# Kernel tuning notes

Hardware: AMD Instinct MI355X
Metric: run time of the kernel (lower is better)

Reference implementation:

```python
import jax, jax.numpy as jnp
import numpy as np

EPS = 1e-5  # torch InstanceNorm2d default eps


def setup_inputs() -> dict:
    key = jax.random.key(0)
    k1, k2, k3, k4, k5 = jax.random.split(key, 5)
    # shapes forced by the module: h*w == 64 (Linear(64,192)), (n,s,c) == (25,128,2)
    inp = jax.random.normal(k1, (25, 2, 128, 8, 8), dtype=jnp.float32)
    qkv_w = jax.random.normal(k2, (192, 64), dtype=jnp.float32) * 0.125
    qkv_b = jax.random.normal(k3, (192,), dtype=jnp.float32) * 0.02
    proj_w = jax.random.normal(k4, (64, 64), dtype=jnp.float32) * 0.125
    proj_b = jax.random.normal(k5, (64,), dtype=jnp.float32) * 0.02
    return {"inp": inp, "qkv_w": qkv_w, "qkv_b": qkv_b,
            "proj_w": proj_w, "proj_b": proj_b}


def reference(inp, qkv_w, qkv_b, proj_w, proj_b):
    n, c, s, h, w = inp.shape  # (25, 2, 128, 8, 8)
    hw = h * w  # 64
    # view(n,c,s,hw).transpose(1,2) -> (n, s, c, hw)
    x = jnp.transpose(inp.reshape(n, c, s, hw), (0, 2, 1, 3))
    # InstanceNorm2d(affine=False): normalize over the last two dims (c, hw)
    # per (n, s) instance, biased variance, eps=1e-5.
    mean = jnp.mean(x, axis=(2, 3), keepdims=True)
    var = jnp.var(x, axis=(2, 3), keepdims=True)
    x = (x - mean) * jax.lax.rsqrt(var + EPS)
    # fused QKV projection on the hw(=64) dim
    qkv = x @ qkv_w.T + qkv_b  # (n, s, c, 192)
    q, k, v = jnp.split(qkv, 3, axis=-1)  # each (n, s, c, 64)
    # linear attention: out = v + q @ (k^T @ v); the 'lower' branch in the
    # original is dead code (never used), so it is omitted.
    kv = jnp.einsum('nscd,nsce->nsde', k, v)  # (n, s, 64, 64)
    attn = v + jnp.einsum('nscd,nsde->nsce', q, kv)  # (n, s, c, 64)
    out = attn @ proj_w.T + proj_b  # dropout is identity in eval mode
    # transpose(1,2).reshape(n,c,s,h,w), residual, final merge of (c,s)
    out = jnp.transpose(out, (0, 2, 1, 3)).reshape(n, c, s, h, w)
    return (out + inp).reshape(n, c * s, h, w)
```

## Files before the change

kernel.cpp:

```cpp
#include <hip/hip_runtime.h>

#define EPS 1e-5f


typedef _Float16 half8 __attribute__((ext_vector_type(8)));
typedef _Float16 half4 __attribute__((ext_vector_type(4)));
typedef float    f32x4 __attribute__((ext_vector_type(4)));

__device__ __forceinline__ int swz(int row, int colByte) {
    return row * 128 + (colByte ^ ((row & 7) << 4));
}

__global__ __launch_bounds__(128)
void attn_mfma(const float* __restrict__ inp,
               const float* __restrict__ qkv_w,
               const float* __restrict__ qkv_b,
               const float* __restrict__ proj_w,
               const float* __restrict__ proj_b,
               float* __restrict__ out)
{
    __shared__ _Float16 w_lds[192 * 64];
    __shared__ _Float16 p_lds[64 * 64];
    __shared__ _Float16 a_lds[32 * 64];

    const int tid = threadIdx.x;
    const int w   = tid >> 6;
    const int l   = tid & 63;
    const int lr  = l & 15;
    const int lg  = l >> 4;

    #pragma unroll
    for (int k = 0; k < 24; ++k) {
        const int idx4 = tid + k * 128;
        const float4 v = reinterpret_cast<const float4*>(qkv_w)[idx4];
        const int row  = idx4 >> 4;
        const int colB = (idx4 & 15) * 8;
        half4 h = { (_Float16)v.x, (_Float16)v.y, (_Float16)v.z, (_Float16)v.w };
        *reinterpret_cast<half4*>(reinterpret_cast<char*>(w_lds) + swz(row, colB)) = h;
    }
    #pragma unroll
    for (int k = 0; k < 8; ++k) {
        const int idx4 = tid + k * 128;
        const float4 v = reinterpret_cast<const float4*>(proj_w)[idx4];
        const int row  = idx4 >> 4;
        const int colB = (idx4 & 15) * 8;
        half4 h = { (_Float16)v.x, (_Float16)v.y, (_Float16)v.z, (_Float16)v.w };
        *reinterpret_cast<half4*>(reinterpret_cast<char*>(p_lds) + swz(row, colB)) = h;
    }

    const int lrow = (w << 4) | lr;
    const int R    = blockIdx.x * 32 + lrow;
    const int g    = R >> 1;
    const int c    = R & 1;
    const int n    = g >> 7;
    const int s    = g & 127;
    const int rowbase = ((n * 2 + c) * 128 + s) * 64;
    const int col0 = lg * 8;

    const float4 x0a = *reinterpret_cast<const float4*>(inp + rowbase + col0);
    const float4 x0b = *reinterpret_cast<const float4*>(inp + rowbase + col0 + 4);
    const float4 x1a = *reinterpret_cast<const float4*>(inp + rowbase + col0 + 32);
    const float4 x1b = *reinterpret_cast<const float4*>(inp + rowbase + col0 + 36);

    float s1 = (x0a.x + x0a.y) + (x0a.z + x0a.w) + (x0b.x + x0b.y) + (x0b.z + x0b.w)
             + (x1a.x + x1a.y) + (x1a.z + x1a.w) + (x1b.x + x1b.y) + (x1b.z + x1b.w);
    float s2 = x0a.x*x0a.x + x0a.y*x0a.y + x0a.z*x0a.z + x0a.w*x0a.w
             + x0b.x*x0b.x + x0b.y*x0b.y + x0b.z*x0b.z + x0b.w*x0b.w
             + x1a.x*x1a.x + x1a.y*x1a.y + x1a.z*x1a.z + x1a.w*x1a.w
             + x1b.x*x1b.x + x1b.y*x1b.y + x1b.z*x1b.z + x1b.w*x1b.w;
    s1 += __shfl_xor(s1, 1);  s2 += __shfl_xor(s2, 1);
    s1 += __shfl_xor(s1, 16); s2 += __shfl_xor(s2, 16);
    s1 += __shfl_xor(s1, 32); s2 += __shfl_xor(s2, 32);
    const float mean = s1 * (1.0f / 128.0f);
    const float var  = s2 * (1.0f / 128.0f) - mean * mean;
    const float rs   = rsqrtf(var + EPS);

    half8 a0, a1;
    a0[0]=(_Float16)((x0a.x-mean)*rs); a0[1]=(_Float16)((x0a.y-mean)*rs);
    a0[2]=(_Float16)((x0a.z-mean)*rs); a0[3]=(_Float16)((x0a.w-mean)*rs);
    a0[4]=(_Float16)((x0b.x-mean)*rs); a0[5]=(_Float16)((x0b.y-mean)*rs);
    a0[6]=(_Float16)((x0b.z-mean)*rs); a0[7]=(_Float16)((x0b.w-mean)*rs);
    a1[0]=(_Float16)((x1a.x-mean)*rs); a1[1]=(_Float16)((x1a.y-mean)*rs);
    a1[2]=(_Float16)((x1a.z-mean)*rs); a1[3]=(_Float16)((x1a.w-mean)*rs);
    a1[4]=(_Float16)((x1b.x-mean)*rs); a1[5]=(_Float16)((x1b.y-mean)*rs);
    a1[6]=(_Float16)((x1b.z-mean)*rs); a1[7]=(_Float16)((x1b.w-mean)*rs);

    __syncthreads();

    f32x4 acc[12];
    #pragma unroll
    for (int nt = 0; nt < 12; ++nt) acc[nt] = f32x4{0.f, 0.f, 0.f, 0.f};

    #pragma unroll
    for (int nt = 0; nt < 12; ++nt) {
        const int o = nt * 16 + lr;
        const half8 b0 = *reinterpret_cast<const half8*>(
            reinterpret_cast<const char*>(w_lds) + swz(o, lg * 16));
        const half8 b1 = *reinterpret_cast<const half8*>(
            reinterpret_cast<const char*>(w_lds) + swz(o, lg * 16 + 64));
        acc[nt] = __builtin_amdgcn_mfma_f32_16x16x32_f16(a0, b0, acc[nt], 0, 0, 0);
        acc[nt] = __builtin_amdgcn_mfma_f32_16x16x32_f16(a1, b1, acc[nt], 0, 0, 0);
    }
    #pragma unroll
    for (int nt = 0; nt < 12; ++nt) {
        const float b = qkv_b[nt * 16 + lr];
        acc[nt].x += b; acc[nt].y += b; acc[nt].z += b; acc[nt].w += b;
    }

    float p[8] = {0.f,0.f,0.f,0.f,0.f,0.f,0.f,0.f};
    #pragma unroll
    for (int nt = 0; nt < 4; ++nt) {
        const f32x4 q = acc[nt], k = acc[4 + nt];
        p[0] = fmaf(q.x, k.x, p[0]);  p[1] = fmaf(q.x, k.y, p[1]);
        p[2] = fmaf(q.y, k.x, p[2]);  p[3] = fmaf(q.y, k.y, p[3]);
        p[4] = fmaf(q.z, k.z, p[4]);  p[5] = fmaf(q.z, k.w, p[5]);
        p[6] = fmaf(q.w, k.z, p[6]);  p[7] = fmaf(q.w, k.w, p[7]);
    }
    #pragma unroll
    for (int m = 8; m >= 1; m >>= 1) {
        #pragma unroll
        for (int z = 0; z < 8; ++z) p[z] += __shfl_xor(p[z], m);
    }
    #pragma unroll
    for (int nt = 0; nt < 4; ++nt) {
        const f32x4 v = acc[8 + nt];
        float av[4];
        av[0] = v.x + fmaf(p[0], v.x, p[1] * v.y);
        av[1] = v.y + fmaf(p[2], v.x, p[3] * v.y);
        av[2] = v.z + fmaf(p[4], v.z, p[5] * v.w);
        av[3] = v.w + fmaf(p[6], v.z, p[7] * v.w);
        #pragma unroll
        for (int r = 0; r < 4; ++r) {
            const int rowl = (w << 4) + lg * 4 + r;
            const int colB = (nt * 16 + lr) * 2;
            *reinterpret_cast<_Float16*>(
                reinterpret_cast<char*>(a_lds) + swz(rowl, colB)) = (_Float16)av[r];
        }
    }
    __syncthreads();

    const half8 a20 = *reinterpret_cast<const half8*>(
        reinterpret_cast<const char*>(a_lds) + swz(lrow, lg * 16));
    const half8 a21 = *reinterpret_cast<const half8*>(
        reinterpret_cast<const char*>(a_lds) + swz(lrow, lg * 16 + 64));
    f32x4 acc2[4];
    #pragma unroll
    for (int nt = 0; nt < 4; ++nt) acc2[nt] = f32x4{0.f, 0.f, 0.f, 0.f};
    #pragma unroll
    for (int nt = 0; nt < 4; ++nt) {
        const int o = nt * 16 + lr;
        const half8 b0 = *reinterpret_cast<const half8*>(
            reinterpret_cast<const char*>(p_lds) + swz(o, lg * 16));
        const half8 b1 = *reinterpret_cast<const half8*>(
            reinterpret_cast<const char*>(p_lds) + swz(o, lg * 16 + 64));
        acc2[nt] = __builtin_amdgcn_mfma_f32_16x16x32_f16(a20, b0, acc2[nt], 0, 0, 0);
        acc2[nt] = __builtin_amdgcn_mfma_f32_16x16x32_f16(a21, b1, acc2[nt], 0, 0, 0);
    }

    #pragma unroll
    for (int nt = 0; nt < 4; ++nt) {
        const int col = nt * 16 + lr;
        const float pb = proj_b[col];
        #pragma unroll
        for (int r = 0; r < 4; ++r) {
            const int Rl = (w << 4) + lg * 4 + r;
            const int Rg = blockIdx.x * 32 + Rl;
            const int gi = Rg >> 1, cc = Rg & 1;
            const int nn = gi >> 7, ss = gi & 127;
            const int addr = ((nn * 2 + cc) * 128 + ss) * 64 + col;
            const float a = (r == 0) ? acc2[nt].x : (r == 1) ? acc2[nt].y
                          : (r == 2) ? acc2[nt].z : acc2[nt].w;
            out[addr] = a + pb + inp[addr];
        }
    }
}

extern "C" void kernel_launch(void* const* d_in, const int* in_sizes, int n_in,
                              void* d_out, int out_size, void* d_ws, size_t ws_size,
                              hipStream_t stream) {
    const float* inp    = (const float*)d_in[0];
    const float* qkv_w  = (const float*)d_in[1];
    const float* qkv_b  = (const float*)d_in[2];
    const float* proj_w = (const float*)d_in[3];
    const float* proj_b = (const float*)d_in[4];
    float* out = (float*)d_out;

    attn_mfma<<<dim3(200), dim3(128), 0, stream>>>(inp, qkv_w, qkv_b, proj_w, proj_b, out);
}
```

Baseline: 9.878 us.

## Load weights directly from global into MFMA operands, single-wave blocks

Drops the cooperative staging of the fp32 QKV and projection weights into LDS. Each lane now reads its weight fragments straight from global memory and converts them to fp16 in registers, which removes the LDS fill and its barrier. The launch moves to 400 blocks of one wavefront each, so more blocks can spread across CUs and each block has less startup work. In exchange every wave re-reads the full weight matrices from L2/L1 and carries more registers for the projection fragments.

```diff
diff --git a/kernel.cpp b/kernel.cpp
--- a/kernel.cpp
+++ b/kernel.cpp
@@ -4,14 +4,20 @@
 
 
 typedef _Float16 half8 __attribute__((ext_vector_type(8)));
-typedef _Float16 half4 __attribute__((ext_vector_type(4)));
 typedef float    f32x4 __attribute__((ext_vector_type(4)));
+
+__device__ __forceinline__ half8 cvt8(float4 a, float4 b) {
+    half8 h;
+    h[0] = (_Float16)a.x; h[1] = (_Float16)a.y; h[2] = (_Float16)a.z; h[3] = (_Float16)a.w;
+    h[4] = (_Float16)b.x; h[5] = (_Float16)b.y; h[6] = (_Float16)b.z; h[7] = (_Float16)b.w;
+    return h;
+}
 
 __device__ __forceinline__ int swz(int row, int colByte) {
     return row * 128 + (colByte ^ ((row & 7) << 4));
 }
 
-__global__ __launch_bounds__(128)
+__global__ __launch_bounds__(64)
 void attn_mfma(const float* __restrict__ inp,
                const float* __restrict__ qkv_w,
                const float* __restrict__ qkv_b,
@@ -19,48 +25,32 @@
                const float* __restrict__ proj_b,
                float* __restrict__ out)
 {
-    __shared__ _Float16 w_lds[192 * 64];
-    __shared__ _Float16 p_lds[64 * 64];
-    __shared__ _Float16 a_lds[32 * 64];
+    __shared__ _Float16 a_lds[16 * 64];
 
-    const int tid = threadIdx.x;
-    const int w   = tid >> 6;
-    const int l   = tid & 63;
-    const int lr  = l & 15;
-    const int lg  = l >> 4;
+    const int l  = threadIdx.x;
+    const int lr = l & 15;
+    const int lg = l >> 4;
 
-    #pragma unroll
-    for (int k = 0; k < 24; ++k) {
-        const int idx4 = tid + k * 128;
-        const float4 v = reinterpret_cast<const float4*>(qkv_w)[idx4];
-        const int row  = idx4 >> 4;
-        const int colB = (idx4 & 15) * 8;
-        half4 h = { (_Float16)v.x, (_Float16)v.y, (_Float16)v.z, (_Float16)v.w };
-        *reinterpret_cast<half4*>(reinterpret_cast<char*>(w_lds) + swz(row, colB)) = h;
-    }
-    #pragma unroll
-    for (int k = 0; k < 8; ++k) {
-        const int idx4 = tid + k * 128;
-        const float4 v = reinterpret_cast<const float4*>(proj_w)[idx4];
-        const int row  = idx4 >> 4;
-        const int colB = (idx4 & 15) * 8;
-        half4 h = { (_Float16)v.x, (_Float16)v.y, (_Float16)v.z, (_Float16)v.w };
-        *reinterpret_cast<half4*>(reinterpret_cast<char*>(p_lds) + swz(row, colB)) = h;
-    }
-
-    const int lrow = (w << 4) | lr;
-    const int R    = blockIdx.x * 32 + lrow;
-    const int g    = R >> 1;
-    const int c    = R & 1;
-    const int n    = g >> 7;
-    const int s    = g & 127;
-    const int rowbase = ((n * 2 + c) * 128 + s) * 64;
+    const int R = blockIdx.x * 16 + lr;
+    const int g = R >> 1, c = R & 1;
+    const int n = g >> 7, s = g & 127;
+    const int rowbase = n * 16384 + c * 8192 + s * 64;
     const int col0 = lg * 8;
 
     const float4 x0a = *reinterpret_cast<const float4*>(inp + rowbase + col0);
     const float4 x0b = *reinterpret_cast<const float4*>(inp + rowbase + col0 + 4);
     const float4 x1a = *reinterpret_cast<const float4*>(inp + rowbase + col0 + 32);
     const float4 x1b = *reinterpret_cast<const float4*>(inp + rowbase + col0 + 36);
+
+    half8 pw0[4], pw1[4];
+    #pragma unroll
+    for (int nt = 0; nt < 4; ++nt) {
+        const float* pb = proj_w + (nt * 16 + lr) * 64 + lg * 8;
+        pw0[nt] = cvt8(*reinterpret_cast<const float4*>(pb),
+                       *reinterpret_cast<const float4*>(pb + 4));
+        pw1[nt] = cvt8(*reinterpret_cast<const float4*>(pb + 32),
+                       *reinterpret_cast<const float4*>(pb + 36));
+    }
 
     float s1 = (x0a.x + x0a.y) + (x0a.z + x0a.w) + (x0b.x + x0b.y) + (x0b.z + x0b.w)
              + (x1a.x + x1a.y) + (x1a.z + x1a.w) + (x1b.x + x1b.y) + (x1b.z + x1b.w);
@@ -85,19 +75,16 @@
     a1[4]=(_Float16)((x1b.x-mean)*rs); a1[5]=(_Float16)((x1b.y-mean)*rs);
     a1[6]=(_Float16)((x1b.z-mean)*rs); a1[7]=(_Float16)((x1b.w-mean)*rs);
 
-    __syncthreads();
-
     f32x4 acc[12];
     #pragma unroll
     for (int nt = 0; nt < 12; ++nt) acc[nt] = f32x4{0.f, 0.f, 0.f, 0.f};
-
     #pragma unroll
     for (int nt = 0; nt < 12; ++nt) {
-        const int o = nt * 16 + lr;
-        const half8 b0 = *reinterpret_cast<const half8*>(
-            reinterpret_cast<const char*>(w_lds) + swz(o, lg * 16));
-        const half8 b1 = *reinterpret_cast<const half8*>(
-            reinterpret_cast<const char*>(w_lds) + swz(o, lg * 16 + 64));
+        const float* wb = qkv_w + (nt * 16 + lr) * 64 + lg * 8;
+        const half8 b0 = cvt8(*reinterpret_cast<const float4*>(wb),
+                              *reinterpret_cast<const float4*>(wb + 4));
+        const half8 b1 = cvt8(*reinterpret_cast<const float4*>(wb + 32),
+                              *reinterpret_cast<const float4*>(wb + 36));
         acc[nt] = __builtin_amdgcn_mfma_f32_16x16x32_f16(a0, b0, acc[nt], 0, 0, 0);
         acc[nt] = __builtin_amdgcn_mfma_f32_16x16x32_f16(a1, b1, acc[nt], 0, 0, 0);
     }
@@ -131,30 +118,25 @@
         av[3] = v.w + fmaf(p[6], v.z, p[7] * v.w);
         #pragma unroll
         for (int r = 0; r < 4; ++r) {
-            const int rowl = (w << 4) + lg * 4 + r;
+            const int row  = lg * 4 + r;
             const int colB = (nt * 16 + lr) * 2;
             *reinterpret_cast<_Float16*>(
-                reinterpret_cast<char*>(a_lds) + swz(rowl, colB)) = (_Float16)av[r];
+                reinterpret_cast<char*>(a_lds) + swz(row, colB)) = (_Float16)av[r];
         }
     }
     __syncthreads();
 
     const half8 a20 = *reinterpret_cast<const half8*>(
-        reinterpret_cast<const char*>(a_lds) + swz(lrow, lg * 16));
+        reinterpret_cast<const char*>(a_lds) + swz(lr, lg * 16));
     const half8 a21 = *reinterpret_cast<const half8*>(
-        reinterpret_cast<const char*>(a_lds) + swz(lrow, lg * 16 + 64));
+        reinterpret_cast<const char*>(a_lds) + swz(lr, lg * 16 + 64));
     f32x4 acc2[4];
     #pragma unroll
     for (int nt = 0; nt < 4; ++nt) acc2[nt] = f32x4{0.f, 0.f, 0.f, 0.f};
     #pragma unroll
     for (int nt = 0; nt < 4; ++nt) {
-        const int o = nt * 16 + lr;
-        const half8 b0 = *reinterpret_cast<const half8*>(
-            reinterpret_cast<const char*>(p_lds) + swz(o, lg * 16));
-        const half8 b1 = *reinterpret_cast<const half8*>(
-            reinterpret_cast<const char*>(p_lds) + swz(o, lg * 16 + 64));
-        acc2[nt] = __builtin_amdgcn_mfma_f32_16x16x32_f16(a20, b0, acc2[nt], 0, 0, 0);
-        acc2[nt] = __builtin_amdgcn_mfma_f32_16x16x32_f16(a21, b1, acc2[nt], 0, 0, 0);
+        acc2[nt] = __builtin_amdgcn_mfma_f32_16x16x32_f16(a20, pw0[nt], acc2[nt], 0, 0, 0);
+        acc2[nt] = __builtin_amdgcn_mfma_f32_16x16x32_f16(a21, pw1[nt], acc2[nt], 0, 0, 0);
     }
 
     #pragma unroll
@@ -163,11 +145,10 @@
         const float pb = proj_b[col];
         #pragma unroll
         for (int r = 0; r < 4; ++r) {
-            const int Rl = (w << 4) + lg * 4 + r;
-            const int Rg = blockIdx.x * 32 + Rl;
+            const int Rg = blockIdx.x * 16 + lg * 4 + r;
             const int gi = Rg >> 1, cc = Rg & 1;
             const int nn = gi >> 7, ss = gi & 127;
-            const int addr = ((nn * 2 + cc) * 128 + ss) * 64 + col;
+            const int addr = nn * 16384 + cc * 8192 + ss * 64 + col;
             const float a = (r == 0) ? acc2[nt].x : (r == 1) ? acc2[nt].y
                           : (r == 2) ? acc2[nt].z : acc2[nt].w;
             out[addr] = a + pb + inp[addr];
@@ -185,5 +166,5 @@
     const float* proj_b = (const float*)d_in[4];
     float* out = (float*)d_out;
 
-    attn_mfma<<<dim3(200), dim3(128), 0, stream>>>(inp, qkv_w, qkv_b, proj_w, proj_b, out);
+    attn_mfma<<<dim3(400), dim3(64), 0, stream>>>(inp, qkv_w, qkv_b, proj_w, proj_b, out);
 }
```

Result: slower. 12.18 us (+23.3%).
